# Kernel tuning notes

Measured on AMD Instinct MI355X. Metric: run time of the kernel, lower is better.

The kernel has to match this reference:

```python
import jax, jax.numpy as jnp
import numpy as np
from jax import lax

NDF = 128
OUT_CH = 256
N_INPUT = 4096
H = W = 64
A_FEAT = OUT_CH * 2 * 2   # 1024
B_OUT = OUT_CH            # 256
C_ROW = 16
BATCH = 128
EPS = 1e-5


def conv2d_s2(x, w):
    # x: NCHW, w: OIHW, stride 2, pad 1 (kernel 4) -> halves spatial dims
    return lax.conv_general_dilated(x, w, window_strides=(2, 2),
                                    padding=[(1, 1), (1, 1)],
                                    dimension_numbers=("NCHW", "OIHW", "NCHW"))


def batchnorm(x, gamma, beta):
    # training-mode batch stats over (N, H, W)
    mean = jnp.mean(x, axis=(0, 2, 3), keepdims=True)
    var = jnp.var(x, axis=(0, 2, 3), keepdims=True)
    xn = (x - mean) * lax.rsqrt(var + EPS)
    return xn * gamma[None, :, None, None] + beta[None, :, None, None]


def lrelu(x):
    return jnp.where(x >= 0, x, 0.2 * x)


def setup_inputs() -> dict:
    key = jax.random.key(0)
    ks = jax.random.split(key, 16)
    s = lambda fan: 1.0 / np.sqrt(fan)
    inp = {
        "image": jax.random.normal(ks[0], (BATCH, 3, H, W), jnp.float32),
        "word_vectors": jax.random.normal(ks[1], (BATCH, N_INPUT), jnp.float32),
        "fc_w": jax.random.normal(ks[2], (H * W, N_INPUT), jnp.float32) * s(N_INPUT),
        "w1": jax.random.normal(ks[3], (NDF, 4, 4, 4), jnp.float32) * s(4 * 16),
        "w2": jax.random.normal(ks[4], (NDF * 2, NDF, 4, 4), jnp.float32) * s(NDF * 16),
        "w3": jax.random.normal(ks[5], (NDF * 2, NDF * 2, 4, 4), jnp.float32) * s(NDF * 2 * 16),
        "w4": jax.random.normal(ks[6], (NDF * 4, NDF * 2, 4, 4), jnp.float32) * s(NDF * 2 * 16),
        "w5": jax.random.normal(ks[7], (OUT_CH, NDF * 4, 4, 4), jnp.float32) * s(NDF * 4 * 16),
        "g2": jnp.ones((NDF * 2,), jnp.float32),
        "b2": jnp.zeros((NDF * 2,), jnp.float32),
        "g3": jnp.ones((NDF * 2,), jnp.float32),
        "b3": jnp.zeros((NDF * 2,), jnp.float32),
        "g4": jnp.ones((NDF * 4,), jnp.float32),
        "b4": jnp.zeros((NDF * 4,), jnp.float32),
        "T": jax.random.uniform(ks[8], (A_FEAT, B_OUT, C_ROW), jnp.float32,
                                 minval=0.0, maxval=1.0 / A_FEAT),
    }
    return inp


def reference(image, word_vectors, fc_w, w1, w2, w3, w4, w5,
              g2, b2, g3, b3, g4, b4, T):
    b = image.shape[0]
    # fc: Linear(no bias) + ReLU (dropout = identity at p=0 / eval)
    wv = jax.nn.relu(word_vectors @ fc_w.T)            # [b, H*W]
    wv = wv.reshape(b, 1, H, W)
    x = jnp.concatenate([image, wv], axis=1)           # [b, 4, 64, 64]
    # conv stack (spectral norm acts on weights; raw weights used here)
    x = lrelu(conv2d_s2(x, w1))                        # [b, ndf, 32, 32]
    x = lrelu(batchnorm(conv2d_s2(x, w2), g2, b2))     # [b, 2ndf, 16, 16]
    x = lrelu(batchnorm(conv2d_s2(x, w3), g3, b3))     # [b, 2ndf, 8, 8]
    x = lrelu(batchnorm(conv2d_s2(x, w4), g4, b4))     # [b, 4ndf, 4, 4]
    x = conv2d_s2(x, w5)                               # [b, out_ch, 2, 2]
    # minibatch discrimination
    feat = x.reshape(b, A_FEAT)                        # [b, 1024]
    Ms = (feat @ T.reshape(A_FEAT, B_OUT * C_ROW)).reshape(b, B_OUT, C_ROW)
    # pairwise L1 over C, exp, sum over batch (including self, as in the loop)
    d = jnp.sum(jnp.abs(Ms[:, None, :, :] - Ms[None, :, :, :]), axis=-1)  # [b,b,B]
    mbd = jnp.sum(jnp.exp(-d), axis=1)                 # [b, B]
    return jnp.concatenate([feat, mbd], axis=1)        # [b, 1280]
```

## Files before the change

### kernel.cpp

```cpp
#include <hip/hip_runtime.h>
#include <cstddef>

#define BB 128

typedef unsigned short u16;
typedef __attribute__((ext_vector_type(8))) short short8;
typedef __attribute__((ext_vector_type(4))) short short4v;
typedef __attribute__((ext_vector_type(4))) float f32x4;

constexpr int ilog2c(int v){ return v<=1 ? 0 : 1+ilog2c(v>>1); }

__device__ __forceinline__ u16 f2b(float f){
  union {float f; unsigned u;} x; x.f = f;
  unsigned u = x.u + 0x7fffu + ((x.u>>16)&1u);
  return (u16)(u>>16);
}
__device__ __forceinline__ float b2f(u16 h){
  union {unsigned u; float f;} x; x.u = ((unsigned)h)<<16;
  return x.f;
}

#define GLOAD_LDS16(gsrc, ldsdst) \
  __builtin_amdgcn_global_load_lds((const __attribute__((address_space(1))) void*)(gsrc), \
      (__attribute__((address_space(3))) void*)(ldsdst), 16, 0, 0)

template<int IC, int OC, int OH, int STORE, int KSPLIT=1>
__global__ __launch_bounds__(512) void convmm2(
    const u16* __restrict__ xp, const u16* __restrict__ wtT, void* __restrict__ yv)
{
  constexpr int OW = OH, S = OH*OW;
  constexpr int IHp = 2*OH+2, IWp = 2*OW+2;
  constexpr int KT = 16*IC;
  constexpr int KTS = KT / KSPLIT;
  constexpr int M = BB * S;
  constexpr int LS = ilog2c(S), LOW = ilog2c(OW), L4 = ilog2c(4*IC);
  __shared__ u16 As[128*64];
  __shared__ u16 Bs[128*64];
  const int tid = threadIdx.x;
  const int n0 = blockIdx.x*128;
  const int m0 = blockIdx.y*128;
  const int kbase = (KSPLIT>1) ? blockIdx.z*KTS : 0;
  const int wave = tid>>6, l = tid&63;
  const int wm = wave>>1, wn = wave&1;

  size_t abase[2]; int au[2];
  #pragma unroll
  for (int t=0;t<2;++t){
    int unit = tid + t*512;
    int r = unit>>3, us = unit&7;
    au[t] = us ^ (r&7);
    int p = m0 + r;
    int b = p >> LS, s = p & (S-1);
    int oh = s >> LOW, ow = s & (OW-1);
    abase[t] = ((size_t)(b*IHp + 2*oh)*IWp + 2*ow)*IC;
  }
  const u16* bsrc[2];
  #pragma unroll
  for (int t=0;t<2;++t){
    int unit = tid + t*512;
    int r = unit>>3, us = unit&7;
    bsrc[t] = wtT + (size_t)(n0+r)*KT + (size_t)(us ^ (r&7))*8;
  }

  f32x4 acc[2][4] = {};

  for (int k0=kbase; k0<kbase+KTS; k0+=64){
    #pragma unroll
    for (int t=0;t<2;++t){
      int k = k0 + au[t]*8;
      int kh = k >> L4, koff = k & (4*IC-1);
      GLOAD_LDS16(xp + abase[t] + (size_t)kh*IWp*IC + koff, &As[(size_t)(t*512 + wave*64)*8]);
    }
    #pragma unroll
    for (int t=0;t<2;++t){
      GLOAD_LDS16(bsrc[t] + k0, &Bs[(size_t)(t*512 + wave*64)*8]);
    }
    __syncthreads();
    #pragma unroll
    for (int kk=0;kk<2;++kk){
      short8 af[2], bfm[4];
      #pragma unroll
      for (int mi=0;mi<2;++mi){
        int row = wm*32 + mi*16 + (l&15);
        int u = (kk*4 + (l>>4)) ^ (row&7);
        af[mi] = *(const short8*)(&As[row*64 + u*8]);
      }
      #pragma unroll
      for (int ni=0;ni<4;++ni){
        int row = wn*64 + ni*16 + (l&15);
        int u = (kk*4 + (l>>4)) ^ (row&7);
        bfm[ni] = *(const short8*)(&Bs[row*64 + u*8]);
      }
      #pragma unroll
      for (int mi=0;mi<2;++mi)
        #pragma unroll
        for (int ni=0;ni<4;++ni)
          acc[mi][ni] = __builtin_amdgcn_mfma_f32_16x16x32_bf16(af[mi], bfm[ni], acc[mi][ni], 0,0,0);
    }
    __syncthreads();
  }
  #pragma unroll
  for (int mi=0;mi<2;++mi){
    #pragma unroll
    for (int ni=0;ni<4;++ni){
      #pragma unroll
      for (int r=0;r<4;++r){
        int row = m0 + wm*32 + mi*16 + (l>>4)*4 + r;
        int col = n0 + wn*64 + ni*16 + (l&15);
        float v = acc[mi][ni][r];
        if (STORE==0){
          ((u16*)yv)[(size_t)row*OC + col] = f2b(v);
        } else if (STORE==1){
          v = v>=0.f ? v : 0.2f*v;
          int b = row>>LS, s = row&(S-1);
          int oh = s>>LOW, ow = s&(OW-1);
          ((u16*)yv)[((size_t)(b*(OH+2) + oh+1)*(OW+2) + ow+1)*OC + col] = f2b(v);
        } else {
          ((float*)yv)[((size_t)blockIdx.z*M + row)*OC + col] = v;
        }
      }
    }
  }
}

template<int B_FP32>
__global__ __launch_bounds__(256) void gemm128_split(
    const u16* __restrict__ A, const void* __restrict__ Bsrc,
    float* __restrict__ part, int K, int kchunk)
{
  __shared__ u16 As[128*64];
  __shared__ u16 Bs[64*64];
  const int tid = threadIdx.x;
  const int n0 = blockIdx.x*64;
  const int kbase = blockIdx.y*kchunk;
  const int wv = tid>>6, l = tid&63;
  f32x4 acc[2][4] = {};
  for (int k0=kbase; k0<kbase+kchunk; k0+=64){
    #pragma unroll
    for (int t=0;t<4;++t){
      int unit = tid + t*256;
      int r = unit>>3, us = unit&7;
      int u = us ^ (r&7);
      *(float4*)(&As[r*64+us*8]) = *(const float4*)(A + (size_t)r*K + k0 + u*8);
    }
    if (B_FP32){
      const float* Bf = (const float*)Bsrc;
      #pragma unroll
      for (int t=0;t<4;++t){
        int unit = tid + t*256;
        int r = unit>>4, u4 = unit&15;
        int u = u4>>1, half = u4&1;
        int us = u ^ (r&7);
        float4 v = *(const float4*)(Bf + (size_t)(n0+r)*K + k0 + u4*4);
        short4v o; o[0]=(short)f2b(v.x); o[1]=(short)f2b(v.y); o[2]=(short)f2b(v.z); o[3]=(short)f2b(v.w);
        *(short4v*)(&Bs[r*64 + us*8 + half*4]) = o;
      }
    } else {
      const u16* Bb = (const u16*)Bsrc;
      #pragma unroll
      for (int t=0;t<2;++t){
        int unit = tid + t*256;
        int r = unit>>3, us = unit&7;
        int u = us ^ (r&7);
        *(float4*)(&Bs[r*64+us*8]) = *(const float4*)(Bb + (size_t)(n0+r)*K + k0 + u*8);
      }
    }
    __syncthreads();
    #pragma unroll
    for (int kk=0;kk<2;++kk){
      short8 af[2], bfm[4];
      #pragma unroll
      for (int mi=0;mi<2;++mi){
        int row = wv*32 + mi*16 + (l&15);
        int u = (kk*4 + (l>>4)) ^ (row&7);
        af[mi] = *(const short8*)(&As[row*64 + u*8]);
      }
      #pragma unroll
      for (int ni=0;ni<4;++ni){
        int row = ni*16 + (l&15);
        int u = (kk*4 + (l>>4)) ^ (row&7);
        bfm[ni] = *(const short8*)(&Bs[row*64 + u*8]);
      }
      #pragma unroll
      for (int mi=0;mi<2;++mi)
        #pragma unroll
        for (int ni=0;ni<4;++ni)
          acc[mi][ni] = __builtin_amdgcn_mfma_f32_16x16x32_bf16(af[mi], bfm[ni], acc[mi][ni], 0,0,0);
    }
    __syncthreads();
  }
  #pragma unroll
  for (int mi=0;mi<2;++mi){
    #pragma unroll
    for (int ni=0;ni<4;++ni){
      #pragma unroll
      for (int r=0;r<4;++r){
        int m = wv*32 + mi*16 + (l>>4)*4 + r;
        int n = n0 + ni*16 + (l&15);
        part[((size_t)blockIdx.y*128 + m)*4096 + n] = acc[mi][ni][r];
      }
    }
  }
}

template<int NS, int STORE>
__global__ __launch_bounds__(256) void reduce_split(const float* __restrict__ part, void* __restrict__ outv)
{
  int idx = blockIdx.x*256 + threadIdx.x;
  float s = 0.f;
  #pragma unroll
  for (int i=0;i<NS;++i) s += part[(size_t)i*524288 + idx];
  if (STORE==0){
    float v = fmaxf(s, 0.f);
    int m = idx>>12, n = idx&4095;
    int h = n>>6, w2 = n&63;
    ((u16*)outv)[((size_t)(m*66 + h+1)*66 + w2+1)*8 + 3] = f2b(v);
  } else {
    ((float*)outv)[idx] = s;
  }
}

template<int NS>
__global__ __launch_bounds__(256) void reduce_part(const float* __restrict__ part,
                                                   u16* __restrict__ out, int total4)
{
  int idx = blockIdx.x*256 + threadIdx.x;
  float4 s = {0.f,0.f,0.f,0.f};
  #pragma unroll
  for (int i=0;i<NS;++i){
    float4 v = *(const float4*)(part + ((size_t)i*total4 + idx)*4);
    s.x+=v.x; s.y+=v.y; s.z+=v.z; s.w+=v.w;
  }
  short4v o; o[0]=(short)f2b(s.x); o[1]=(short)f2b(s.y); o[2]=(short)f2b(s.z); o[3]=(short)f2b(s.w);
  *(short4v*)(out + (size_t)idx*4) = o;
}

__global__ __launch_bounds__(256) void conv5_reduce(const float* __restrict__ part,
                                                    float* __restrict__ out, u16* __restrict__ featb)
{
  int idx = blockIdx.x*256 + threadIdx.x;
  float s = 0.f;
  #pragma unroll
  for (int i=0;i<32;++i) s += part[(size_t)i*131072 + idx];
  int row = idx>>8, col = idx&255;
  int b = row>>2, sp = row&3;
  out[(size_t)b*1280 + col*4 + sp] = s;
  featb[(size_t)b*1024 + col*4 + sp] = f2b(s);
}

template<int IC, int ICP>
__device__ __forceinline__ void repack_dev(const float* __restrict__ w, u16* __restrict__ wt,
                                           int oc, int tid, float* ls){
  for (int i=tid; i<IC*16; i+=256){
    int ic = i>>4, khkw = i&15;
    ls[ic*17+khkw] = w[(size_t)oc*IC*16 + i];
  }
  __syncthreads();
  constexpr int KT = 16*ICP;
  constexpr int LP = ilog2c(ICP);
  for (int k=tid; k<KT; k+=256){
    int khkw = k >> LP, ic = k & (ICP-1);
    float v = (ic<IC) ? ls[ic*17+khkw] : 0.f;
    wt[(size_t)oc*KT + k] = f2b(v);
  }
}

__device__ __forceinline__ void transpose_dev(const float* __restrict__ T, u16* __restrict__ Tt,
                                              int idx, int tid, float* tile){
  int bx = idx & 127, by = idx >> 7;
  int kb = by*32, nb = bx*32;
  int tx = tid&31, ty = tid>>5;
  #pragma unroll
  for (int i=0;i<32;i+=8)
    tile[(ty+i)*33 + tx] = T[(size_t)(kb+ty+i)*4096 + nb+tx];
  __syncthreads();
  #pragma unroll
  for (int i=0;i<32;i+=8)
    Tt[(size_t)(nb+ty+i)*1024 + kb+tx] = f2b(tile[tx*33 + ty+i]);
}

__global__ __launch_bounds__(256) void prep_all(
    const float* __restrict__ w1, const float* __restrict__ w2, const float* __restrict__ w3,
    const float* __restrict__ w4, const float* __restrict__ w5, const float* __restrict__ T,
    const float* __restrict__ wvec,
    u16* wt1T, u16* wt2T, u16* wt3T, u16* wt4T, u16* wt5T, u16* Tt, u16* wvb)
{
  __shared__ float ls[512*17];
  const int blk = blockIdx.x, tid = threadIdx.x;
  if (blk < 128)        repack_dev<4,8>(w1, wt1T, blk, tid, ls);
  else if (blk < 384)   repack_dev<128,128>(w2, wt2T, blk-128, tid, ls);
  else if (blk < 640)   repack_dev<256,256>(w3, wt3T, blk-384, tid, ls);
  else if (blk < 1152)  repack_dev<256,256>(w4, wt4T, blk-640, tid, ls);
  else if (blk < 1408)  repack_dev<512,512>(w5, wt5T, blk-1152, tid, ls);
  else if (blk < 5504)  transpose_dev(T, Tt, blk-1408, tid, ls);
  else { int i = (blk-5504)*256 + tid; wvb[i] = f2b(wvec[i]); }
}

template<int Hp, int C>
__device__ __forceinline__ void zb_border(u16* __restrict__ buf, int idx, int count){
  if (idx >= count) return;
  constexpr int NP = 4*Hp - 4;
  constexpr int PC = NP*C;
  int b = idx / PC;
  int rem = idx - b*PC;
  int p = rem >> ilog2c(C);
  int c = rem & (C-1);
  int h, w;
  if (p < Hp){ h = 0; w = p; }
  else if (p < 2*Hp){ h = Hp-1; w = p - Hp; }
  else { int q = p - 2*Hp; h = 1 + (q>>1); w = (q&1) ? (Hp-1) : 0; }
  buf[(((size_t)b*Hp + h)*Hp + w)*C + c] = 0;
}

__global__ __launch_bounds__(256) void zb_early(u16* xp0, u16* xp1, u16* xp2){
  const int blk = blockIdx.x, tid = threadIdx.x;
  if (blk < 2178){
    int i = blk*256 + tid;
    if (i < 557568){ short8 z = {}; *(short8*)(xp0 + (size_t)i*8) = z; }
  } else if (blk < 10626){
    zb_border<34,128>(xp1, (blk-2178)*256 + tid, 2162688);
  } else {
    zb_border<18,256>(xp2, (blk-10626)*256 + tid, 2228224);
  }
}

__global__ __launch_bounds__(256) void zb_late(u16* xp3, u16* xp4){
  const int blk = blockIdx.x, tid = threadIdx.x;
  if (blk < 4608) zb_border<10,256>(xp3, blk*256 + tid, 1179648);
  else            zb_border<6,512>(xp4, (blk-4608)*256 + tid, 1310720);
}

__global__ __launch_bounds__(256) void pack_x0(const float* __restrict__ img, u16* __restrict__ xp0){
  int idx = blockIdx.x*256+threadIdx.x;
  int b = idx>>12, s = idx&4095;
  int h = s>>6, w = s&63;
  u16* d = xp0 + ((size_t)(b*66 + h+1)*66 + w+1)*8;
  d[0] = f2b(img[(size_t)(b*3+0)*4096 + s]);
  d[1] = f2b(img[(size_t)(b*3+1)*4096 + s]);
  d[2] = f2b(img[(size_t)(b*3+2)*4096 + s]);
}

template<int C>
__global__ __launch_bounds__(256) void bn_stats2(const u16* __restrict__ y, float* __restrict__ stats, int Mblk){
  constexpr int CU = C/8, NR = 256/CU, LCU = ilog2c(CU);
  __shared__ float red[NR*C];
  const int cu = threadIdx.x & (CU-1);
  const int rg = threadIdx.x >> LCU;
  const int base = blockIdx.x*Mblk;
  float s[8] = {}, ss[8] = {};
  for (int p = base+rg; p < base+Mblk; p += NR){
    short8 v = *(const short8*)(y + (size_t)p*C + cu*8);
    #pragma unroll
    for (int j=0;j<8;++j){ float f=b2f((u16)v[j]); s[j]+=f; ss[j]+=f*f; }
  }
  #pragma unroll
  for (int j=0;j<8;++j) red[rg*C + cu*8 + j] = s[j];
  __syncthreads();
  for (int c=threadIdx.x; c<C; c+=256){
    float t=0.f;
    #pragma unroll
    for (int r2=0;r2<NR;++r2) t += red[r2*C+c];
    stats[blockIdx.x*512 + c] = t;
  }
  __syncthreads();
  #pragma unroll
  for (int j=0;j<8;++j) red[rg*C + cu*8 + j] = ss[j];
  __syncthreads();
  for (int c=threadIdx.x; c<C; c+=256){
    float t=0.f;
    #pragma unroll
    for (int r2=0;r2<NR;++r2) t += red[r2*C+c];
    stats[131072 + blockIdx.x*512 + c] = t;
  }
}

template<int C>
__global__ __launch_bounds__(C) void bn_finalize(float* __restrict__ stats, const float* __restrict__ g,
                                                 const float* __restrict__ be, float cnt){
  int c = threadIdx.x;
  float s=0.f, ss=0.f;
  for (int b=0;b<256;++b){ s += stats[b*512+c]; ss += stats[131072 + b*512+c]; }
  float m = s/cnt;
  float var = ss/cnt - m*m;
  float A = rsqrtf(var + 1e-5f)*g[c];
  stats[262144 + c] = A;
  stats[262144 + 512 + c] = be[c] - m*A;
}

template<int C, int OH>
__global__ __launch_bounds__(256) void bn_apply(const u16* __restrict__ y, const float* __restrict__ stats,
                                                u16* __restrict__ xp){
  constexpr int S = OH*OH, LS = ilog2c(S), LOW = ilog2c(OH);
  constexpr int CU = C/8, LCU = ilog2c(CU);
  int idx = blockIdx.x*256 + threadIdx.x;
  int p = idx >> LCU, cu = idx & (CU-1);
  short8 v8 = *(const short8*)(y + (size_t)p*C + cu*8);
  const float* Ap = stats + 262144;
  const float* Bp = stats + 262144 + 512;
  u16 o[8];
  #pragma unroll
  for (int j=0;j<8;++j){
    float v = b2f((u16)v8[j])*Ap[cu*8+j] + Bp[cu*8+j];
    o[j] = f2b(v>=0.f ? v : 0.2f*v);
  }
  int b = p>>LS, s = p&(S-1), oh = s>>LOW, ow = s&(OH-1);
  *(short8*)(xp + ((size_t)(b*(OH+2)+oh+1)*(OH+2)+ow+1)*C + cu*8) = *(short8*)o;
}

__global__ __launch_bounds__(256) void mbd_kernel(
    const float* __restrict__ Ms, float* __restrict__ out)
{
  const int i = blockIdx.x;
  const int o = threadIdx.x;
  float mi[16];
  #pragma unroll
  for (int u = 0; u < 4; ++u) {
    float4 v = *(const float4*)&Ms[(size_t)i * 4096 + o * 16 + u * 4];
    mi[u*4+0]=v.x; mi[u*4+1]=v.y; mi[u*4+2]=v.z; mi[u*4+3]=v.w;
  }
  float acc = 0.f;
  for (int j = 0; j < BB; ++j) {
    float d = 0.f;
    #pragma unroll
    for (int u = 0; u < 4; ++u) {
      float4 v = *(const float4*)&Ms[(size_t)j * 4096 + o * 16 + u * 4];
      d += fabsf(mi[u*4+0]-v.x) + fabsf(mi[u*4+1]-v.y) + fabsf(mi[u*4+2]-v.z) + fabsf(mi[u*4+3]-v.w);
    }
    acc += expf(-d);
  }
  out[(size_t)i * 1280 + 1024 + o] = acc;
}

__global__ void ws_too_small(float* out, int n){
  int idx = blockIdx.x*256+threadIdx.x;
  if (idx<n) out[idx] = -777.0f;
}

extern "C" void kernel_launch(void* const* d_in, const int* in_sizes, int n_in,
                              void* d_out, int out_size, void* d_ws, size_t ws_size,
                              hipStream_t stream)
{
  const float* image = (const float*)d_in[0];
  const float* wvec  = (const float*)d_in[1];
  const float* fc_w  = (const float*)d_in[2];
  const float* w1    = (const float*)d_in[3];
  const float* w2    = (const float*)d_in[4];
  const float* w3    = (const float*)d_in[5];
  const float* w4    = (const float*)d_in[6];
  const float* w5    = (const float*)d_in[7];
  const float* g2    = (const float*)d_in[8];
  const float* b2    = (const float*)d_in[9];
  const float* g3    = (const float*)d_in[10];
  const float* b3    = (const float*)d_in[11];
  const float* g4    = (const float*)d_in[12];
  const float* b4    = (const float*)d_in[13];
  const float* T     = (const float*)d_in[14];
  float* out = (float*)d_out;
  char* wsb = (char*)d_ws;

  const size_t NEED = 105816064ull;
  if (ws_size < NEED) {
    ws_too_small<<<(out_size + 255)/256, 256, 0, stream>>>(out, out_size);
    return;
  }

  u16* xp1   = (u16*)(wsb + 0);
  u16* y3    = (u16*)(wsb + 0);
  u16* xp3   = (u16*)(wsb + 4194304);
  u16* y4    = (u16*)(wsb + 10747904);
  u16* xp4   = (u16*)(wsb + 12845056);
  float* Ms  = (float*)(wsb + 17563648);
  u16* featb = (u16*)(wsb + 19660800);
  float* stats = (float*)(wsb + 19922944);
  u16* xp2   = (u16*)(wsb + 37879808);
  float* c4part = (float*)(wsb + 37879808);
  float* c5part = (float*)(wsb + 37879808);
  u16* y2    = (u16*)(wsb + 59113472);
  float* gpart  = (float*)(wsb + 59113472);
  float* c3part = (float*)(wsb + 59113472);
  u16* xp0   = (u16*)(wsb + 75890688);
  u16* wt1T  = (u16*)(wsb + 84811776);
  u16* wt2T  = (u16*)(wsb + 84844544);
  u16* wt3T  = (u16*)(wsb + 85893120);
  u16* wt4T  = (u16*)(wsb + 87990272);
  u16* wt5T  = (u16*)(wsb + 92184576);
  u16* Tt    = (u16*)(wsb + 96378880);
  u16* wvb   = (u16*)(wsb + 104767488);

  zb_early<<<19330, 256, 0, stream>>>(xp0, xp1, xp2);
  prep_all<<<7552, 256, 0, stream>>>(w1, w2, w3, w4, w5, T, wvec,
                                     wt1T, wt2T, wt3T, wt4T, wt5T, Tt, wvb);

  gemm128_split<1><<<dim3(64,8), 256, 0, stream>>>(wvb, fc_w, gpart, 4096, 512);
  reduce_split<8,0><<<2048, 256, 0, stream>>>(gpart, xp0);
  pack_x0<<<2048, 256, 0, stream>>>(image, xp0);

  convmm2<8,128,32,1><<<dim3(1,1024), 512, 0, stream>>>(xp0, wt1T, xp1);
  convmm2<128,256,16,0><<<dim3(2,256), 512, 0, stream>>>(xp1, wt2T, y2);

  zb_late<<<9728, 256, 0, stream>>>(xp3, xp4);

  bn_stats2<256><<<256, 256, 0, stream>>>(y2, stats, 128);
  bn_finalize<256><<<1, 256, 0, stream>>>(stats, g2, b2, 32768.f);
  bn_apply<256,16><<<4096, 256, 0, stream>>>(y2, stats, xp2);

  convmm2<256,256,8,3,2><<<dim3(2,64,2), 512, 0, stream>>>(xp2, wt3T, c3part);
  reduce_part<2><<<2048, 256, 0, stream>>>(c3part, y3, 524288);
  bn_stats2<256><<<256, 256, 0, stream>>>(y3, stats, 32);
  bn_finalize<256><<<1, 256, 0, stream>>>(stats, g3, b3, 8192.f);
  bn_apply<256,8><<<1024, 256, 0, stream>>>(y3, stats, xp3);

  convmm2<256,512,4,3,4><<<dim3(4,16,4), 512, 0, stream>>>(xp3, wt4T, c4part);
  reduce_part<4><<<1024, 256, 0, stream>>>(c4part, y4, 262144);
  bn_stats2<512><<<256, 256, 0, stream>>>(y4, stats, 8);
  bn_finalize<512><<<1, 512, 0, stream>>>(stats, g4, b4, 2048.f);
  bn_apply<512,4><<<512, 256, 0, stream>>>(y4, stats, xp4);

  convmm2<512,256,2,3,32><<<dim3(2,4,32), 512, 0, stream>>>(xp4, wt5T, c5part);
  conv5_reduce<<<512, 256, 0, stream>>>(c5part, out, featb);

  gemm128_split<0><<<dim3(64,8), 256, 0, stream>>>(featb, Tt, gpart, 1024, 128);
  reduce_split<8,1><<<2048, 256, 0, stream>>>(gpart, Ms);
  mbd_kernel<<<128, 256, 0, stream>>>(Ms, out);
}
```

Baseline: 295.4 us.

## Double-buffer conv and GEMM LDS tiles, fuse split reduction with BN stats

```diff
diff --git a/kernel.cpp b/kernel.cpp
--- a/kernel.cpp
+++ b/kernel.cpp
@@ -32,10 +32,11 @@
   constexpr int IHp = 2*OH+2, IWp = 2*OW+2;
   constexpr int KT = 16*IC;
   constexpr int KTS = KT / KSPLIT;
+  constexpr int NT = KTS / 64;
   constexpr int M = BB * S;
   constexpr int LS = ilog2c(S), LOW = ilog2c(OW), L4 = ilog2c(4*IC);
-  __shared__ u16 As[128*64];
-  __shared__ u16 Bs[128*64];
+  __shared__ u16 As[2*128*64];
+  __shared__ u16 Bs[2*128*64];
   const int tid = threadIdx.x;
   const int n0 = blockIdx.x*128;
   const int m0 = blockIdx.y*128;
@@ -62,20 +63,27 @@
     bsrc[t] = wtT + (size_t)(n0+r)*KT + (size_t)(us ^ (r&7))*8;
   }
 
-  f32x4 acc[2][4] = {};
-
-  for (int k0=kbase; k0<kbase+KTS; k0+=64){
+  auto stage = [&](int half, int k0){
     #pragma unroll
     for (int t=0;t<2;++t){
       int k = k0 + au[t]*8;
       int kh = k >> L4, koff = k & (4*IC-1);
-      GLOAD_LDS16(xp + abase[t] + (size_t)kh*IWp*IC + koff, &As[(size_t)(t*512 + wave*64)*8]);
+      GLOAD_LDS16(xp + abase[t] + (size_t)kh*IWp*IC + koff,
+                  &As[half*8192 + (size_t)(t*512 + wave*64)*8]);
     }
     #pragma unroll
     for (int t=0;t<2;++t){
-      GLOAD_LDS16(bsrc[t] + k0, &Bs[(size_t)(t*512 + wave*64)*8]);
-    }
-    __syncthreads();
+      GLOAD_LDS16(bsrc[t] + k0, &Bs[half*8192 + (size_t)(t*512 + wave*64)*8]);
+    }
+  };
+
+  f32x4 acc[2][4] = {};
+
+  stage(0, kbase);
+  __syncthreads();
+  int cur = 0;
+  for (int t=0; t<NT; ++t){
+    if (t+1 < NT) stage(cur^1, kbase + (t+1)*64);
     #pragma unroll
     for (int kk=0;kk<2;++kk){
       short8 af[2], bfm[4];
@@ -83,13 +91,13 @@
       for (int mi=0;mi<2;++mi){
         int row = wm*32 + mi*16 + (l&15);
         int u = (kk*4 + (l>>4)) ^ (row&7);
-        af[mi] = *(const short8*)(&As[row*64 + u*8]);
+        af[mi] = *(const short8*)(&As[cur*8192 + row*64 + u*8]);
       }
       #pragma unroll
       for (int ni=0;ni<4;++ni){
         int row = wn*64 + ni*16 + (l&15);
         int u = (kk*4 + (l>>4)) ^ (row&7);
-        bfm[ni] = *(const short8*)(&Bs[row*64 + u*8]);
+        bfm[ni] = *(const short8*)(&Bs[cur*8192 + row*64 + u*8]);
       }
       #pragma unroll
       for (int mi=0;mi<2;++mi)
@@ -98,6 +106,7 @@
           acc[mi][ni] = __builtin_amdgcn_mfma_f32_16x16x32_bf16(af[mi], bfm[ni], acc[mi][ni], 0,0,0);
     }
     __syncthreads();
+    cur ^= 1;
   }
   #pragma unroll
   for (int mi=0;mi<2;++mi){
@@ -123,63 +132,56 @@
   }
 }
 
-template<int B_FP32>
 __global__ __launch_bounds__(256) void gemm128_split(
-    const u16* __restrict__ A, const void* __restrict__ Bsrc,
+    const u16* __restrict__ A, const u16* __restrict__ B,
     float* __restrict__ part, int K, int kchunk)
 {
-  __shared__ u16 As[128*64];
-  __shared__ u16 Bs[64*64];
+  __shared__ u16 As[2*128*64];
+  __shared__ u16 Bs[2*64*64];
   const int tid = threadIdx.x;
   const int n0 = blockIdx.x*64;
   const int kbase = blockIdx.y*kchunk;
-  const int wv = tid>>6, l = tid&63;
+  const int wave = tid>>6, l = tid&63;
+  const u16* asrc[4]; const u16* bsrc[2];
+  #pragma unroll
+  for (int t=0;t<4;++t){
+    int unit = tid + t*256, r = unit>>3, us = unit&7;
+    asrc[t] = A + (size_t)r*K + (size_t)(us ^ (r&7))*8;
+  }
+  #pragma unroll
+  for (int t=0;t<2;++t){
+    int unit = tid + t*256, r = unit>>3, us = unit&7;
+    bsrc[t] = B + (size_t)(n0+r)*K + (size_t)(us ^ (r&7))*8;
+  }
+  auto stage = [&](int half, int k0){
+    #pragma unroll
+    for (int t=0;t<4;++t)
+      GLOAD_LDS16(asrc[t] + k0, &As[half*8192 + (size_t)(t*256 + wave*64)*8]);
+    #pragma unroll
+    for (int t=0;t<2;++t)
+      GLOAD_LDS16(bsrc[t] + k0, &Bs[half*4096 + (size_t)(t*256 + wave*64)*8]);
+  };
   f32x4 acc[2][4] = {};
-  for (int k0=kbase; k0<kbase+kchunk; k0+=64){
-    #pragma unroll
-    for (int t=0;t<4;++t){
-      int unit = tid + t*256;
-      int r = unit>>3, us = unit&7;
-      int u = us ^ (r&7);
-      *(float4*)(&As[r*64+us*8]) = *(const float4*)(A + (size_t)r*K + k0 + u*8);
-    }
-    if (B_FP32){
-      const float* Bf = (const float*)Bsrc;
-      #pragma unroll
-      for (int t=0;t<4;++t){
-        int unit = tid + t*256;
-        int r = unit>>4, u4 = unit&15;
-        int u = u4>>1, half = u4&1;
-        int us = u ^ (r&7);
-        float4 v = *(const float4*)(Bf + (size_t)(n0+r)*K + k0 + u4*4);
-        short4v o; o[0]=(short)f2b(v.x); o[1]=(short)f2b(v.y); o[2]=(short)f2b(v.z); o[3]=(short)f2b(v.w);
-        *(short4v*)(&Bs[r*64 + us*8 + half*4]) = o;
-      }
-    } else {
-      const u16* Bb = (const u16*)Bsrc;
-      #pragma unroll
-      for (int t=0;t<2;++t){
-        int unit = tid + t*256;
-        int r = unit>>3, us = unit&7;
-        int u = us ^ (r&7);
-        *(float4*)(&Bs[r*64+us*8]) = *(const float4*)(Bb + (size_t)(n0+r)*K + k0 + u*8);
-      }
-    }
-    __syncthreads();
+  const int NT = kchunk >> 6;
+  stage(0, kbase);
+  __syncthreads();
+  int cur = 0;
+  for (int t=0;t<NT;++t){
+    if (t+1 < NT) stage(cur^1, kbase + (t+1)*64);
     #pragma unroll
     for (int kk=0;kk<2;++kk){
       short8 af[2], bfm[4];
       #pragma unroll
       for (int mi=0;mi<2;++mi){
-        int row = wv*32 + mi*16 + (l&15);
+        int row = wave*32 + mi*16 + (l&15);
         int u = (kk*4 + (l>>4)) ^ (row&7);
-        af[mi] = *(const short8*)(&As[row*64 + u*8]);
+        af[mi] = *(const short8*)(&As[cur*8192 + row*64 + u*8]);
       }
       #pragma unroll
       for (int ni=0;ni<4;++ni){
         int row = ni*16 + (l&15);
         int u = (kk*4 + (l>>4)) ^ (row&7);
-        bfm[ni] = *(const short8*)(&Bs[row*64 + u*8]);
+        bfm[ni] = *(const short8*)(&Bs[cur*4096 + row*64 + u*8]);
       }
       #pragma unroll
       for (int mi=0;mi<2;++mi)
@@ -188,6 +190,7 @@
           acc[mi][ni] = __builtin_amdgcn_mfma_f32_16x16x32_bf16(af[mi], bfm[ni], acc[mi][ni], 0,0,0);
     }
     __syncthreads();
+    cur ^= 1;
   }
   #pragma unroll
   for (int mi=0;mi<2;++mi){
@@ -195,7 +198,7 @@
     for (int ni=0;ni<4;++ni){
       #pragma unroll
       for (int r=0;r<4;++r){
-        int m = wv*32 + mi*16 + (l>>4)*4 + r;
+        int m = wave*32 + mi*16 + (l>>4)*4 + r;
         int n = n0 + ni*16 + (l&15);
         part[((size_t)blockIdx.y*128 + m)*4096 + n] = acc[mi][ni][r];
       }
@@ -220,19 +223,57 @@
   }
 }
 
-template<int NS>
-__global__ __launch_bounds__(256) void reduce_part(const float* __restrict__ part,
-                                                   u16* __restrict__ out, int total4)
-{
-  int idx = blockIdx.x*256 + threadIdx.x;
-  float4 s = {0.f,0.f,0.f,0.f};
-  #pragma unroll
-  for (int i=0;i<NS;++i){
-    float4 v = *(const float4*)(part + ((size_t)i*total4 + idx)*4);
-    s.x+=v.x; s.y+=v.y; s.z+=v.z; s.w+=v.w;
-  }
-  short4v o; o[0]=(short)f2b(s.x); o[1]=(short)f2b(s.y); o[2]=(short)f2b(s.z); o[3]=(short)f2b(s.w);
-  *(short4v*)(out + (size_t)idx*4) = o;
+template<int NS, int C>
+__global__ __launch_bounds__(256) void reduce_bn(
+    const float* __restrict__ part, u16* __restrict__ y,
+    float* __restrict__ stats, int Mblk, int Mtot)
+{
+  constexpr int CU = C/8, NR = 256/CU, LCU = ilog2c(CU);
+  __shared__ float red[NR*C];
+  const int cu = threadIdx.x & (CU-1);
+  const int rg = threadIdx.x >> LCU;
+  const int base = blockIdx.x*Mblk;
+  float s[8] = {}, ss[8] = {};
+  for (int p = base+rg; p < base+Mblk; p += NR){
+    float a8[8];
+    #pragma unroll
+    for (int j=0;j<8;++j) a8[j]=0.f;
+    #pragma unroll
+    for (int i=0;i<NS;++i){
+      const float* src = part + ((size_t)i*Mtot + p)*C + cu*8;
+      float4 v0 = *(const float4*)src;
+      float4 v1 = *(const float4*)(src+4);
+      a8[0]+=v0.x; a8[1]+=v0.y; a8[2]+=v0.z; a8[3]+=v0.w;
+      a8[4]+=v1.x; a8[5]+=v1.y; a8[6]+=v1.z; a8[7]+=v1.w;
+    }
+    u16 o[8];
+    #pragma unroll
+    for (int j=0;j<8;++j){
+      o[j] = f2b(a8[j]);
+      float vb = b2f(o[j]);
+      s[j]+=vb; ss[j]+=vb*vb;
+    }
+    *(short8*)(y + (size_t)p*C + cu*8) = *(short8*)o;
+  }
+  #pragma unroll
+  for (int j=0;j<8;++j) red[rg*C + cu*8 + j] = s[j];
+  __syncthreads();
+  for (int c=threadIdx.x; c<C; c+=256){
+    float t=0.f;
+    #pragma unroll
+    for (int r2=0;r2<NR;++r2) t += red[r2*C+c];
+    stats[blockIdx.x*512 + c] = t;
+  }
+  __syncthreads();
+  #pragma unroll
+  for (int j=0;j<8;++j) red[rg*C + cu*8 + j] = ss[j];
+  __syncthreads();
+  for (int c=threadIdx.x; c<C; c+=256){
+    float t=0.f;
+    #pragma unroll
+    for (int r2=0;r2<NR;++r2) t += red[r2*C+c];
+    stats[131072 + blockIdx.x*512 + c] = t;
+  }
 }
 
 __global__ __launch_bounds__(256) void conv5_reduce(const float* __restrict__ part,
@@ -282,8 +323,8 @@
 __global__ __launch_bounds__(256) void prep_all(
     const float* __restrict__ w1, const float* __restrict__ w2, const float* __restrict__ w3,
     const float* __restrict__ w4, const float* __restrict__ w5, const float* __restrict__ T,
-    const float* __restrict__ wvec,
-    u16* wt1T, u16* wt2T, u16* wt3T, u16* wt4T, u16* wt5T, u16* Tt, u16* wvb)
+    const float* __restrict__ wvec, const float* __restrict__ fc_w,
+    u16* wt1T, u16* wt2T, u16* wt3T, u16* wt4T, u16* wt5T, u16* Tt, u16* wvb, u16* fcw_b)
 {
   __shared__ float ls[512*17];
   const int blk = blockIdx.x, tid = threadIdx.x;
@@ -293,7 +334,13 @@
   else if (blk < 1152)  repack_dev<256,256>(w4, wt4T, blk-640, tid, ls);
   else if (blk < 1408)  repack_dev<512,512>(w5, wt5T, blk-1152, tid, ls);
   else if (blk < 5504)  transpose_dev(T, Tt, blk-1408, tid, ls);
-  else { int i = (blk-5504)*256 + tid; wvb[i] = f2b(wvec[i]); }
+  else if (blk < 7552){ int i = (blk-5504)*256 + tid; wvb[i] = f2b(wvec[i]); }
+  else {
+    int i = (blk-7552)*256 + tid;
+    float4 v = ((const float4*)fc_w)[i];
+    short4v o; o[0]=(short)f2b(v.x); o[1]=(short)f2b(v.y); o[2]=(short)f2b(v.z); o[3]=(short)f2b(v.w);
+    *(short4v*)(fcw_b + (size_t)i*4) = o;
+  }
 }
 
 template<int Hp, int C>
@@ -314,14 +361,9 @@
 
 __global__ __launch_bounds__(256) void zb_early(u16* xp0, u16* xp1, u16* xp2){
   const int blk = blockIdx.x, tid = threadIdx.x;
-  if (blk < 2178){
-    int i = blk*256 + tid;
-    if (i < 557568){ short8 z = {}; *(short8*)(xp0 + (size_t)i*8) = z; }
-  } else if (blk < 10626){
-    zb_border<34,128>(xp1, (blk-2178)*256 + tid, 2162688);
-  } else {
-    zb_border<18,256>(xp2, (blk-10626)*256 + tid, 2228224);
-  }
+  if (blk < 1040)       zb_border<66,8>(xp0, blk*256 + tid, 266240);
+  else if (blk < 9488)  zb_border<34,128>(xp1, (blk-1040)*256 + tid, 2162688);
+  else                  zb_border<18,256>(xp2, (blk-9488)*256 + tid, 2228224);
 }
 
 __global__ __launch_bounds__(256) void zb_late(u16* xp3, u16* xp4){
@@ -334,10 +376,11 @@
   int idx = blockIdx.x*256+threadIdx.x;
   int b = idx>>12, s = idx&4095;
   int h = s>>6, w = s&63;
-  u16* d = xp0 + ((size_t)(b*66 + h+1)*66 + w+1)*8;
-  d[0] = f2b(img[(size_t)(b*3+0)*4096 + s]);
-  d[1] = f2b(img[(size_t)(b*3+1)*4096 + s]);
-  d[2] = f2b(img[(size_t)(b*3+2)*4096 + s]);
+  short8 o = {};
+  o[0] = (short)f2b(img[(size_t)(b*3+0)*4096 + s]);
+  o[1] = (short)f2b(img[(size_t)(b*3+1)*4096 + s]);
+  o[2] = (short)f2b(img[(size_t)(b*3+2)*4096 + s]);
+  *(short8*)(xp0 + ((size_t)(b*66 + h+1)*66 + w+1)*8) = o;
 }
 
 template<int C>
@@ -464,6 +507,7 @@
     return;
   }
 
+  u16* fcw_b = (u16*)(wsb + 0);
   u16* xp1   = (u16*)(wsb + 0);
   u16* y3    = (u16*)(wsb + 0);
   u16* xp3   = (u16*)(wsb + 4194304);
@@ -487,13 +531,14 @@
   u16* Tt    = (u16*)(wsb + 96378880);
   u16* wvb   = (u16*)(wsb + 104767488);
 
-  zb_early<<<19330, 256, 0, stream>>>(xp0, xp1, xp2);
-  prep_all<<<7552, 256, 0, stream>>>(w1, w2, w3, w4, w5, T, wvec,
-                                     wt1T, wt2T, wt3T, wt4T, wt5T, Tt, wvb);
-
-  gemm128_split<1><<<dim3(64,8), 256, 0, stream>>>(wvb, fc_w, gpart, 4096, 512);
+  prep_all<<<23936, 256, 0, stream>>>(w1, w2, w3, w4, w5, T, wvec, fc_w,
+                                      wt1T, wt2T, wt3T, wt4T, wt5T, Tt, wvb, fcw_b);
+  pack_x0<<<2048, 256, 0, stream>>>(image, xp0);
+
+  gemm128_split<<<dim3(64,8), 256, 0, stream>>>(wvb, fcw_b, gpart, 4096, 512);
   reduce_split<8,0><<<2048, 256, 0, stream>>>(gpart, xp0);
-  pack_x0<<<2048, 256, 0, stream>>>(image, xp0);
+
+  zb_early<<<18192, 256, 0, stream>>>(xp0, xp1, xp2);
 
   convmm2<8,128,32,1><<<dim3(1,1024), 512, 0, stream>>>(xp0, wt1T, xp1);
   convmm2<128,256,16,0><<<dim3(2,256), 512, 0, stream>>>(xp1, wt2T, y2);
@@ -505,21 +550,19 @@
   bn_apply<256,16><<<4096, 256, 0, stream>>>(y2, stats, xp2);
 
   convmm2<256,256,8,3,2><<<dim3(2,64,2), 512, 0, stream>>>(xp2, wt3T, c3part);
-  reduce_part<2><<<2048, 256, 0, stream>>>(c3part, y3, 524288);
-  bn_stats2<256><<<256, 256, 0, stream>>>(y3, stats, 32);
+  reduce_bn<2,256><<<256, 256, 0, stream>>>(c3part, y3, stats, 32, 8192);
   bn_finalize<256><<<1, 256, 0, stream>>>(stats, g3, b3, 8192.f);
   bn_apply<256,8><<<1024, 256, 0, stream>>>(y3, stats, xp3);
 
   convmm2<256,512,4,3,4><<<dim3(4,16,4), 512, 0, stream>>>(xp3, wt4T, c4part);
-  reduce_part<4><<<1024, 256, 0, stream>>>(c4part, y4, 262144);
-  bn_stats2<512><<<256, 256, 0, stream>>>(y4, stats, 8);
+  reduce_bn<4,512><<<256, 256, 0, stream>>>(c4part, y4, stats, 8, 2048);
   bn_finalize<512><<<1, 512, 0, stream>>>(stats, g4, b4, 2048.f);
   bn_apply<512,4><<<512, 256, 0, stream>>>(y4, stats, xp4);
 
   convmm2<512,256,2,3,32><<<dim3(2,4,32), 512, 0, stream>>>(xp4, wt5T, c5part);
   conv5_reduce<<<512, 256, 0, stream>>>(c5part, out, featb);
 
-  gemm128_split<0><<<dim3(64,8), 256, 0, stream>>>(featb, Tt, gpart, 1024, 128);
+  gemm128_split<<<dim3(64,8), 256, 0, stream>>>(featb, Tt, gpart, 1024, 128);
   reduce_split<8,1><<<2048, 256, 0, stream>>>(gpart, Ms);
   mbd_kernel<<<128, 256, 0, stream>>>(Ms, out);
 }
```

New measurement: 302.2 us. +2.3%, slower.
